# Kernel optimization log

Measured on AMD Instinct MI355X. Metric: run time of the kernel, lower is better.

The kernel has to match this reference:

```python
import jax, jax.numpy as jnp
import numpy as np

N, E, F, HID, PC, HEADS = 100000, 1600000, 128, 128, 16, 4
RATIO = 0.8
NEG_SLOPE = 0.2
BIG_NEG = -1e9


def setup_inputs() -> dict:
    ks = jax.random.split(jax.random.key(0), 20)
    def g(k, shape, fan):
        return jax.random.normal(k, shape, jnp.float32) / np.float32(np.sqrt(fan))
    return {
        "x": jax.random.normal(ks[0], (N, F), jnp.float32),
        "edge_index": jax.random.randint(ks[1], (2, E), 0, N, dtype=jnp.int32),
        "edge_attr": jax.random.uniform(ks[2], (E, 1), dtype=jnp.float32),
        "W1": g(ks[3], (F, PC), F),
        "att_src1": g(ks[4], (HEADS, PC // HEADS), PC // HEADS),
        "att_dst1": g(ks[5], (HEADS, PC // HEADS), PC // HEADS),
        "We1": g(ks[6], (1, PC), 1),
        "att_edge1": g(ks[7], (HEADS, PC // HEADS), PC // HEADS),
        "b1": jnp.zeros((PC,), jnp.float32),
        "Wrel": g(ks[8], (PC, 1), PC),
        "brel": jnp.zeros((1,), jnp.float32),
        "Wroot": g(ks[9], (PC, 1), PC),
        "W2": g(ks[10], (PC, HID), PC),
        "att_src2": g(ks[11], (1, HID), HID),
        "att_dst2": g(ks[12], (1, HID), HID),
        "We2": g(ks[13], (1, HID), 1),
        "att_edge2": g(ks[14], (1, HID), HID),
        "b2": jnp.zeros((HID,), jnp.float32),
        "Wg": g(ks[15], (HID, 1), HID),
        "bg": jnp.zeros((1,), jnp.float32),
    }


def gat_conv(h_in, src, dst, e_attr, W, a_s, a_d, We, a_e, b, num_nodes, mask=None):
    """PyG GATConv (add_self_loops=False, eval-mode so dropout is identity)."""
    H, D = a_s.shape
    h = (h_in @ W).reshape(-1, H, D)                      # [N,H,D]
    al_s = jnp.einsum('nhd,hd->nh', h, a_s)               # alpha contribution of source
    al_d = jnp.einsum('nhd,hd->nh', h, a_d)               # alpha contribution of dest
    he = (e_attr @ We).reshape(-1, H, D)                  # [E,H,D] edge features
    al_e = jnp.einsum('ehd,hd->eh', he, a_e)              # [E,H]
    logits = jax.nn.leaky_relu(al_s[src] + al_d[dst] + al_e, NEG_SLOPE)  # [E,H]
    if mask is not None:
        logits = jnp.where(mask[:, None], logits, BIG_NEG)
    # segment softmax over incoming edges of each destination node
    m = jnp.maximum(jax.ops.segment_max(logits, dst, num_segments=num_nodes), BIG_NEG)
    num = jnp.exp(logits - m[dst])
    if mask is not None:
        num = jnp.where(mask[:, None], num, 0.0)
    den = jax.ops.segment_sum(num, dst, num_segments=num_nodes)
    coef = num / jnp.maximum(den[dst], 1e-16)             # [E,H]
    out = jax.ops.segment_sum(coef[:, :, None] * h[src], dst, num_segments=num_nodes)
    return out.reshape(num_nodes, H * D) + b


def _forward(x, edge_attr, W1, att_src1, att_dst1, We1, att_edge1, b1,
             Wrel, brel, Wroot, W2, att_src2, att_dst2, We2, att_edge2, b2,
             Wg, bg, edge_index):
    n = x.shape[0]
    src, dst = edge_index[0], edge_index[1]
    h1 = jax.nn.relu(gat_conv(x, src, dst, edge_attr, W1, att_src1, att_dst1, We1, att_edge1, b1, n))
    # --- SAGPooling: GraphConv score -> tanh -> top-k -> masked subgraph (n > node_threshold always) ---
    agg = jax.ops.segment_sum(h1[src], dst, num_segments=n)           # neighbor sum
    score = (agg @ Wrel + brel + h1 @ Wroot).reshape(-1)              # GraphConv(16 -> 1)
    k = int(np.ceil(RATIO * n))                                       # static
    vals, perm = jax.lax.top_k(score, k)
    new_idx = jnp.full((n,), -1, dtype=jnp.int32).at[perm].set(jnp.arange(k, dtype=jnp.int32))
    src_n, dst_n = new_idx[src], new_idx[dst]
    emask = (src_n >= 0) & (dst_n >= 0)                               # edges with both ends kept
    src2 = jnp.where(emask, src_n, 0)
    dst2 = jnp.where(emask, dst_n, 0)
    x2 = h1[perm] * jnp.tanh(vals)[:, None]                           # gate kept nodes
    h2 = jax.nn.relu(gat_conv(x2, src2, dst2, edge_attr, W2, att_src2, att_dst2, We2, att_edge2, b2, k, mask=emask))
    # --- AttentionalAggregation + MaxAggregation over the single graph (index = zeros) ---
    gate = jax.nn.softmax(h2 @ Wg + bg, axis=0)                       # [k,1]
    att = (gate * h2).sum(axis=0, keepdims=True)                      # [1,HID]
    mx = h2.max(axis=0, keepdims=True)                                # [1,HID]
    return jnp.concatenate([att, mx], axis=1)                         # [1,2*HID]


def reference(x, edge_index, edge_attr, W1, att_src1, att_dst1, We1, att_edge1, b1,
              Wrel, brel, Wroot, W2, att_src2, att_dst2, We2, att_edge2, b2, Wg, bg):
    return _forward(x, edge_attr, W1, att_src1, att_dst1, We1, att_edge1, b1,
                    Wrel, brel, Wroot, W2, att_src2, att_dst2, We2, att_edge2, b2,
                    Wg, bg, edge_index)
```

## Files before the change

### kernel.cpp

```cpp
#include <hip/hip_runtime.h>
#include <hip/hip_bf16.h>

#define Nn 100000
#define Ee 1600000
#define Kk 80000
#define NB ((Nn + 255) / 256)
#define NBK 196
#define CHK 8192
#define G2B 2048

typedef unsigned int uint;
typedef unsigned short ushort;

struct Scal {
    uint prefix, remaining, needEq;
    float c1[4];
    float c2;
    uint gmaxOrd;
    float deng;
    float attnum[128];
    uint mxOrd[128];
};

__device__ __forceinline__ uint f2ord(float f) {
    uint b = __float_as_uint(f);
    return (b & 0x80000000u) ? ~b : (b | 0x80000000u);
}
__device__ __forceinline__ float ord2f(uint u) {
    uint b = (u & 0x80000000u) ? (u ^ 0x80000000u) : ~u;
    return __uint_as_float(b);
}
__device__ __forceinline__ float lrelu(float v) { return v > 0.f ? v : 0.2f * v; }
__device__ __forceinline__ float2 bf2f2(uint u) {
    return make_float2(__uint_as_float(u << 16), __uint_as_float(u & 0xFFFF0000u));
}

__global__ __launch_bounds__(256) void initK(uint* bcnt, uint* hist, Scal* sc,
                                             const float* We1, const float* ae1,
                                             const float* We2, const float* ae2) {
    int i = blockIdx.x * 256 + threadIdx.x;
    if (i < NBK) bcnt[i] = 0u;
    if (i < 256) hist[i] = 0u;
    if (i < 128) { sc->attnum[i] = 0.f; sc->mxOrd[i] = f2ord(0.0f); }
    if (i == 0) {
        sc->prefix = 0u; sc->remaining = Kk; sc->needEq = 0u;
        sc->deng = 0.f; sc->gmaxOrd = f2ord(-1e30f);
        for (int h = 0; h < 4; h++) {
            float s = 0.f;
            for (int d = 0; d < 4; d++) s += We1[h * 4 + d] * ae1[h * 4 + d];
            sc->c1[h] = s;
        }
        float s2 = 0.f;
        for (int d = 0; d < 128; d++) s2 += We2[d] * ae2[d];
        sc->c2 = s2;
    }
}

__global__ __launch_bounds__(256) void nodeL1(const float* __restrict__ x,
                                              const float* __restrict__ W1,
                                              const float* __restrict__ as1,
                                              const float* __restrict__ ad1,
                                              float* __restrict__ hpre,
                                              float* __restrict__ alS1,
                                              float* __restrict__ alD1) {
    __shared__ float Ws[128 * 16];
    __shared__ float s_as[16], s_ad[16];
    for (int i = threadIdx.x; i < 2048; i += 256) Ws[i] = W1[i];
    if (threadIdx.x < 16) { s_as[threadIdx.x] = as1[threadIdx.x]; s_ad[threadIdx.x] = ad1[threadIdx.x]; }
    __syncthreads();
    int n = blockIdx.x * 256 + threadIdx.x;
    if (n >= Nn) return;
    float acc[16];
#pragma unroll
    for (int j = 0; j < 16; j++) acc[j] = 0.f;
    const float4* xr = (const float4*)(x + (size_t)n * 128);
    for (int t4 = 0; t4 < 32; t4++) {
        float4 xv = xr[t4];
#pragma unroll
        for (int j = 0; j < 16; j++) {
            acc[j] += xv.x * Ws[(t4 * 4 + 0) * 16 + j];
            acc[j] += xv.y * Ws[(t4 * 4 + 1) * 16 + j];
            acc[j] += xv.z * Ws[(t4 * 4 + 2) * 16 + j];
            acc[j] += xv.w * Ws[(t4 * 4 + 3) * 16 + j];
        }
    }
    float* hp = hpre + (size_t)n * 16;
#pragma unroll
    for (int j = 0; j < 16; j++) hp[j] = acc[j];
#pragma unroll
    for (int h = 0; h < 4; h++) {
        float s = 0.f, d = 0.f;
#pragma unroll
        for (int q = 0; q < 4; q++) {
            s += acc[h * 4 + q] * s_as[h * 4 + q];
            d += acc[h * 4 + q] * s_ad[h * 4 + q];
        }
        alS1[n * 4 + h] = s;
        alD1[n * 4 + h] = d;
    }
}

__global__ __launch_bounds__(256) void bucketCnt(const int* __restrict__ ei, uint* __restrict__ bcnt) {
    __shared__ uint h[NBK];
    if (threadIdx.x < NBK) h[threadIdx.x] = 0u;
    __syncthreads();
    for (int e = blockIdx.x * 256 + threadIdx.x; e < Ee; e += gridDim.x * 256)
        atomicAdd(&h[((uint)ei[Ee + e]) >> 9], 1u);
    __syncthreads();
    if (threadIdx.x < NBK && h[threadIdx.x]) atomicAdd(&bcnt[threadIdx.x], h[threadIdx.x]);
}

__global__ __launch_bounds__(256) void scanBk(const uint* __restrict__ bcnt, uint* __restrict__ boff,
                                              uint* __restrict__ gcur) {
    __shared__ uint s[256];
    int t = threadIdx.x;
    uint v = (t < NBK) ? bcnt[t] : 0u;
    s[t] = v;
    __syncthreads();
    for (int off = 1; off < 256; off <<= 1) {
        uint u = (t >= off) ? s[t - off] : 0u;
        __syncthreads();
        s[t] += u;
        __syncthreads();
    }
    if (t < NBK) { boff[t] = s[t] - v; gcur[t] = 0u; }
    if (t == 0) boff[NBK] = Ee;
}

__global__ __launch_bounds__(256) void binScat(const int* __restrict__ ei, const float* __restrict__ ea,
                                               const uint* __restrict__ boff, uint* __restrict__ gcur,
                                               uint2* __restrict__ bsE, ushort* __restrict__ bsD) {
    __shared__ uint h[NBK], base[NBK], h2[NBK];
    int t = threadIdx.x;
    if (t < NBK) h[t] = 0u;
    __syncthreads();
    int estart = blockIdx.x * CHK;
    int eend = min(Ee, estart + CHK);
    for (int e = estart + t; e < eend; e += 256)
        atomicAdd(&h[((uint)ei[Ee + e]) >> 9], 1u);
    __syncthreads();
    if (t < NBK) { base[t] = atomicAdd(&gcur[t], h[t]); h2[t] = 0u; }
    __syncthreads();
    for (int e = estart + t; e < eend; e += 256) {
        uint d = (uint)ei[Ee + e];
        uint b = d >> 9;
        uint r = atomicAdd(&h2[b], 1u);
        uint pos = boff[b] + base[b] + r;
        bsE[pos] = make_uint2((uint)ei[e], __float_as_uint(ea[e]));
        bsD[pos] = (ushort)(d & 511u);
    }
}

__global__ __launch_bounds__(256) void rankK(const uint* __restrict__ boff, const ushort* __restrict__ bsD,
                                             ushort* __restrict__ bsR, uint* __restrict__ deg) {
    __shared__ uint ldeg[512];
    int b = blockIdx.x, t = threadIdx.x;
    ldeg[t] = 0u; ldeg[t + 256] = 0u;
    __syncthreads();
    uint r0 = boff[b], r1 = boff[b + 1];
    for (uint i = r0 + t; i < r1; i += 256)
        bsR[i] = (ushort)atomicAdd(&ldeg[bsD[i]], 1u);
    __syncthreads();
    int nd = b * 512 + t;
    if (nd < Nn) deg[nd] = ldeg[t];
    nd = b * 512 + 256 + t;
    if (nd < Nn) deg[nd] = ldeg[256 + t];
}

__global__ __launch_bounds__(256) void scanA(const uint* __restrict__ deg, uint* __restrict__ rowstart,
                                             uint* __restrict__ blkSum) {
    __shared__ uint s[256];
    int i = blockIdx.x * 256 + threadIdx.x;
    uint v = (i < Nn) ? deg[i] : 0u;
    s[threadIdx.x] = v;
    __syncthreads();
    for (int off = 1; off < 256; off <<= 1) {
        uint t = (threadIdx.x >= off) ? s[threadIdx.x - off] : 0u;
        __syncthreads();
        s[threadIdx.x] += t;
        __syncthreads();
    }
    if (i < Nn) rowstart[i] = s[threadIdx.x] - v;
    if (threadIdx.x == 255) blkSum[blockIdx.x] = s[255];
}

__global__ __launch_bounds__(512) void scanB(const uint* __restrict__ blkSum, uint* __restrict__ blkOff) {
    __shared__ uint s[512];
    uint v = (threadIdx.x < NB) ? blkSum[threadIdx.x] : 0u;
    s[threadIdx.x] = v;
    __syncthreads();
    for (int off = 1; off < 512; off <<= 1) {
        uint t = (threadIdx.x >= off) ? s[threadIdx.x - off] : 0u;
        __syncthreads();
        s[threadIdx.x] += t;
        __syncthreads();
    }
    if (threadIdx.x < NB) blkOff[threadIdx.x] = s[threadIdx.x] - v;
}

__global__ __launch_bounds__(256) void scanC(uint* __restrict__ rowstart, const uint* __restrict__ blkOff) {
    int i = blockIdx.x * 256 + threadIdx.x;
    if (i < Nn) rowstart[i] += blkOff[blockIdx.x];
    if (i == 0) rowstart[Nn] = Ee;
}

__global__ __launch_bounds__(256) void placeK(const uint* __restrict__ boff, const uint2* __restrict__ bsE,
                                              const ushort* __restrict__ bsD, const ushort* __restrict__ bsR,
                                              const uint* __restrict__ rowstart, uint2* __restrict__ csr_p8) {
    __shared__ uint srs[512];
    int b = blockIdx.x, t = threadIdx.x;
    int nd = b * 512 + t;
    srs[t] = (nd < Nn) ? rowstart[nd] : 0u;
    nd = b * 512 + 256 + t;
    srs[256 + t] = (nd < Nn) ? rowstart[nd] : 0u;
    __syncthreads();
    uint r0 = boff[b], r1 = boff[b + 1];
    for (uint i = r0 + t; i < r1; i += 256)
        csr_p8[srs[bsD[i]] + bsR[i]] = bsE[i];
}

__global__ __launch_bounds__(256) void gather1f(const uint2* __restrict__ csr_p8,
                                                const uint* __restrict__ rowstart,
                                                const float* __restrict__ alS1, const float* __restrict__ alD1,
                                                const float* __restrict__ hpre, const Scal* __restrict__ scc,
                                                const float* __restrict__ b1, const float* __restrict__ Wrel,
                                                const float* __restrict__ Wroot,
                                                float* __restrict__ h1, float* __restrict__ p,
                                                float* __restrict__ q) {
    int tid = blockIdx.x * 256 + threadIdx.x;
    if (tid >= Nn * 4) return;
    int d = tid >> 2, h = tid & 3;
    uint r0 = rowstart[d], r1 = rowstart[d + 1];
    float ad = alD1[tid];
    float c1h = scc->c1[h];
    float den = 0.f;
    float4 acc = {0.f, 0.f, 0.f, 0.f};
#pragma unroll 8
    for (uint i = r0; i < r1; i++) {
        uint2 p8 = csr_p8[i];
        int s = (int)p8.x;
        float e = __expf(lrelu(alS1[s * 4 + h] + __uint_as_float(p8.y) * c1h + ad));
        float4 hv = *(const float4*)(hpre + (size_t)s * 16 + h * 4);
        den += e;
        acc.x += e * hv.x; acc.y += e * hv.y;
        acc.z += e * hv.z; acc.w += e * hv.w;
    }
    float inv = 1.f / fmaxf(den, 1e-16f);
    float4 o;
    o.x = fmaxf(acc.x * inv + b1[h * 4 + 0], 0.f);
    o.y = fmaxf(acc.y * inv + b1[h * 4 + 1], 0.f);
    o.z = fmaxf(acc.z * inv + b1[h * 4 + 2], 0.f);
    o.w = fmaxf(acc.w * inv + b1[h * 4 + 3], 0.f);
    *(float4*)(h1 + (size_t)d * 16 + h * 4) = o;
    float pp = o.x * Wrel[h * 4 + 0] + o.y * Wrel[h * 4 + 1] + o.z * Wrel[h * 4 + 2] + o.w * Wrel[h * 4 + 3];
    float qq = o.x * Wroot[h * 4 + 0] + o.y * Wroot[h * 4 + 1] + o.z * Wroot[h * 4 + 2] + o.w * Wroot[h * 4 + 3];
    pp += __shfl_xor(pp, 1); pp += __shfl_xor(pp, 2);
    qq += __shfl_xor(qq, 1); qq += __shfl_xor(qq, 2);
    if (h == 0) { p[d] = pp; q[d] = qq; }
}

__global__ __launch_bounds__(256) void scoreK2(const uint2* __restrict__ csr_p8, const uint* __restrict__ rowstart,
                                               const float* __restrict__ p, const float* __restrict__ q,
                                               const float* __restrict__ brel,
                                               float* __restrict__ score, uint* __restrict__ dkey) {
    int d = blockIdx.x * 256 + threadIdx.x;
    if (d >= Nn) return;
    uint r0 = rowstart[d], r1 = rowstart[d + 1];
    float s = brel[0] + q[d];
#pragma unroll 8
    for (uint i = r0; i < r1; i++) s += p[(int)csr_p8[i].x];
    score[d] = s;
    dkey[d] = ~f2ord(s);
}

__global__ __launch_bounds__(256) void histK(const uint* __restrict__ dkey, const Scal* __restrict__ sc,
                                             uint* __restrict__ hist, int shift) {
    __shared__ uint lh[256];
    lh[threadIdx.x] = 0u;
    __syncthreads();
    int i = blockIdx.x * 256 + threadIdx.x;
    if (i < Nn) {
        uint d = dkey[i];
        bool ok = (shift == 24) || ((d >> (shift + 8)) == sc->prefix);
        if (ok) atomicAdd(&lh[(d >> shift) & 255u], 1u);
    }
    __syncthreads();
    if (lh[threadIdx.x]) atomicAdd(&hist[threadIdx.x], lh[threadIdx.x]);
}

__global__ __launch_bounds__(256) void selP(Scal* sc, uint* hist) {
    __shared__ uint s[256];
    int t = threadIdx.x;
    uint c = hist[t];
    s[t] = c;
    __syncthreads();
    for (int off = 1; off < 256; off <<= 1) {
        uint v = (t >= off) ? s[t - off] : 0u;
        __syncthreads();
        s[t] += v;
        __syncthreads();
    }
    uint rem = sc->remaining;
    uint cum = s[t];
    uint cumex = cum - c;
    if (cum >= rem && cumex < rem) {
        sc->remaining = rem - cumex;
        sc->prefix = (sc->prefix << 8) | (uint)t;
    }
    hist[t] = 0u;
}

__global__ __launch_bounds__(256) void cntK(const uint* __restrict__ dkey, const Scal* __restrict__ sc,
                                            uint* __restrict__ blkLt, uint* __restrict__ blkEq) {
    int i = blockIdx.x * 256 + threadIdx.x;
    uint ut = sc->prefix;
    bool lt = (i < Nn) && (dkey[i] < ut);
    bool eq = (i < Nn) && (dkey[i] == ut);
    __shared__ uint sl[4], se[4];
    unsigned long long bl = __ballot(lt), be = __ballot(eq);
    int lane = threadIdx.x & 63, w = threadIdx.x >> 6;
    if (lane == 0) { sl[w] = (uint)__popcll(bl); se[w] = (uint)__popcll(be); }
    __syncthreads();
    if (threadIdx.x == 0) {
        blkLt[blockIdx.x] = sl[0] + sl[1] + sl[2] + sl[3];
        blkEq[blockIdx.x] = se[0] + se[1] + se[2] + se[3];
    }
}

__global__ __launch_bounds__(512) void prefP(Scal* sc, const uint* __restrict__ blkLt,
                                             const uint* __restrict__ blkEq, uint* __restrict__ eqPref) {
    __shared__ uint se[512];
    __shared__ uint sl[512];
    int t = threadIdx.x;
    uint e = (t < NB) ? blkEq[t] : 0u;
    uint l = (t < NB) ? blkLt[t] : 0u;
    se[t] = e; sl[t] = l;
    __syncthreads();
    for (int off = 1; off < 512; off <<= 1) {
        uint v1 = (t >= off) ? se[t - off] : 0u;
        uint v2 = (t >= off) ? sl[t - off] : 0u;
        __syncthreads();
        se[t] += v1; sl[t] += v2;
        __syncthreads();
    }
    if (t < NB) eqPref[t] = se[t] - e;
    if (t == 511) sc->needEq = Kk - sl[511];
}

__global__ __launch_bounds__(256) void keptK(const uint* __restrict__ dkey, const Scal* __restrict__ sc,
                                             const uint* __restrict__ eqPref, int* __restrict__ kept) {
    int i = blockIdx.x * 256 + threadIdx.x;
    uint ut = sc->prefix, needEq = sc->needEq;
    bool inr = i < Nn;
    uint d = inr ? dkey[i] : 0xFFFFFFFFu;
    bool isLt = inr && (d < ut);
    bool isEq = inr && (d == ut);
    __shared__ uint wcnt[4];
    unsigned long long mask = __ballot(isEq);
    int lane = threadIdx.x & 63, w = threadIdx.x >> 6;
    uint lanePre = (uint)__popcll(mask & ((1ull << lane) - 1ull));
    if (lane == 0) wcnt[w] = (uint)__popcll(mask);
    __syncthreads();
    uint wo = 0;
    for (int q = 0; q < 4; q++) if (q < w) wo += wcnt[q];
    uint rank = eqPref[blockIdx.x] + wo + lanePre;
    if (inr) kept[i] = (isLt || (isEq && rank < needEq)) ? 1 : 0;
}

__global__ __launch_bounds__(256) void nodeL2(const float* __restrict__ h1, const float* __restrict__ score,
                                              const int* __restrict__ kept, const float* __restrict__ W2,
                                              const float* __restrict__ as2, const float* __restrict__ ad2,
                                              __hip_bfloat162* __restrict__ h2b, float* __restrict__ alS2k,
                                              float* __restrict__ alD2) {
    __shared__ float Ws[16 * 128];
    for (int i = threadIdx.x; i < 2048; i += 256) Ws[i] = W2[i];
    __syncthreads();
    int wid = (blockIdx.x * 256 + threadIdx.x) >> 6;
    int lane = threadIdx.x & 63;
    if (wid >= Nn) return;
    int n = wid;
    if (!kept[n]) { if (lane == 0) alS2k[n] = -1e30f; return; }
    float t = tanhf(score[n]);
    float x2[16];
    const float* hr = h1 + (size_t)n * 16;
#pragma unroll
    for (int j = 0; j < 16; j++) x2[j] = hr[j] * t;
    int d0 = 2 * lane, d1 = 2 * lane + 1;
    float a0 = 0.f, a1 = 0.f;
    const float2* Wv = (const float2*)Ws;
#pragma unroll
    for (int j = 0; j < 16; j++) {
        float2 wv = Wv[j * 64 + lane];
        a0 += x2[j] * wv.x;
        a1 += x2[j] * wv.y;
    }
    __hip_bfloat162 hb;
    hb.x = __float2bfloat16(a0);
    hb.y = __float2bfloat16(a1);
    h2b[(size_t)n * 64 + lane] = hb;
    float s = a0 * as2[d0] + a1 * as2[d1];
    float dd = a0 * ad2[d0] + a1 * ad2[d1];
#pragma unroll
    for (int off = 32; off; off >>= 1) { s += __shfl_xor(s, off); dd += __shfl_xor(dd, off); }
    if (lane == 0) { alS2k[n] = s; alD2[n] = dd; }
}

__global__ __launch_bounds__(256) void gather2g(const uint2* __restrict__ csr_p8,
                                                const uint* __restrict__ rowstart, const int* __restrict__ kept,
                                                const float* __restrict__ alS2k, const float* __restrict__ alD2,
                                                const Scal* __restrict__ scc,
                                                const __hip_bfloat162* __restrict__ h2b, const float* __restrict__ b2,
                                                const float* __restrict__ Wg, const float* __restrict__ bg,
                                                float* __restrict__ pacc, float* __restrict__ pmx,
                                                float* __restrict__ pden) {
    __shared__ float sAtt[4][16][8];
    __shared__ float sMx[4][16][8];
    __shared__ float sDen[4];
    int w = threadIdx.x >> 6, lane = threadIdx.x & 63;
    int g = lane >> 4, t = lane & 15;
    float4 b2a = ((const float4*)b2)[t * 2], b2b = ((const float4*)b2)[t * 2 + 1];
    float4 wga = ((const float4*)Wg)[t * 2], wgb = ((const float4*)Wg)[t * 2 + 1];
    float bg0 = bg[0];
    float c2 = scc->c2;
    const uint* h2u = (const uint*)h2b;
    float att[8], mx8[8], denP = 0.f;
#pragma unroll
    for (int j = 0; j < 8; j++) { att[j] = 0.f; mx8[j] = 0.f; }
    for (int n = blockIdx.x * 4 + w; n < Nn; n += G2B * 4) {
        if (!kept[n]) continue;
        float ad = alD2[n];
        uint r0 = rowstart[n];
        uint len = rowstart[n + 1] - r0;
        float den = 0.f;
        float acc[8];
#pragma unroll
        for (int d = 0; d < 8; d++) acc[d] = 0.f;
#pragma unroll 2
        for (uint base = 0; base < len; base += 4) {
            uint off = base + (uint)g;
            bool act = off < len;
            uint sidx = act ? (r0 + off) : (r0 + len - 1);
            uint2 p8 = csr_p8[sidx];
            int s = (int)p8.x;
            float pv = alS2k[s] + __uint_as_float(p8.y) * c2;
            pv = act ? pv : -1e30f;
            float c = __expf(lrelu(pv + ad));
            uint4 hv = *(const uint4*)(h2u + (size_t)s * 64 + t * 4);
            den += c;
            float2 f;
            f = bf2f2(hv.x); acc[0] += c * f.x; acc[1] += c * f.y;
            f = bf2f2(hv.y); acc[2] += c * f.x; acc[3] += c * f.y;
            f = bf2f2(hv.z); acc[4] += c * f.x; acc[5] += c * f.y;
            f = bf2f2(hv.w); acc[6] += c * f.x; acc[7] += c * f.y;
        }
#pragma unroll
        for (int d = 0; d < 8; d++) {
            acc[d] += __shfl_xor(acc[d], 16);
            acc[d] += __shfl_xor(acc[d], 32);
        }
        den += __shfl_xor(den, 16);
        den += __shfl_xor(den, 32);
        float inv = 1.f / fmaxf(den, 1e-16f);
        float o[8];
        o[0] = fmaxf(acc[0] * inv + b2a.x, 0.f);
        o[1] = fmaxf(acc[1] * inv + b2a.y, 0.f);
        o[2] = fmaxf(acc[2] * inv + b2a.z, 0.f);
        o[3] = fmaxf(acc[3] * inv + b2a.w, 0.f);
        o[4] = fmaxf(acc[4] * inv + b2b.x, 0.f);
        o[5] = fmaxf(acc[5] * inv + b2b.y, 0.f);
        o[6] = fmaxf(acc[6] * inv + b2b.z, 0.f);
        o[7] = fmaxf(acc[7] * inv + b2b.w, 0.f);
        float gp = o[0] * wga.x + o[1] * wga.y + o[2] * wga.z + o[3] * wga.w +
                   o[4] * wgb.x + o[5] * wgb.y + o[6] * wgb.z + o[7] * wgb.w;
#pragma unroll
        for (int off = 8; off; off >>= 1) gp += __shfl_xor(gp, off);
        float e = __expf(gp + bg0);
        denP += e;
#pragma unroll
        for (int j = 0; j < 8; j++) {
            att[j] += e * o[j];
            mx8[j] = fmaxf(mx8[j], o[j]);
        }
    }
    if (g == 0) {
#pragma unroll
        for (int j = 0; j < 8; j++) { sAtt[w][t][j] = att[j]; sMx[w][t][j] = mx8[j]; }
    }
    if (lane == 0) sDen[w] = denP;
    __syncthreads();
    int tid = threadIdx.x;
    if (tid < 128) {
        int tt = tid >> 3, j = tid & 7;
        float a = sAtt[0][tt][j] + sAtt[1][tt][j] + sAtt[2][tt][j] + sAtt[3][tt][j];
        float m = fmaxf(fmaxf(sMx[0][tt][j], sMx[1][tt][j]), fmaxf(sMx[2][tt][j], sMx[3][tt][j]));
        pacc[(size_t)blockIdx.x * 128 + tid] = a;
        pmx[(size_t)blockIdx.x * 128 + tid] = m;
    }
    if (tid == 0) pden[blockIdx.x] = sDen[0] + sDen[1] + sDen[2] + sDen[3];
}

__global__ __launch_bounds__(256) void gateRed(const float* __restrict__ pacc, const float* __restrict__ pmx,
                                               const float* __restrict__ pden, Scal* sc) {
    __shared__ float r[256];
    int b = blockIdx.x, tid = threadIdx.x;
    if (b < 128) {
        float a = 0.f, m = 0.f;
        for (int i = tid; i < G2B; i += 256) {
            a += pacc[(size_t)i * 128 + b];
            m = fmaxf(m, pmx[(size_t)i * 128 + b]);
        }
        r[tid] = a;
        __syncthreads();
        for (int off = 128; off; off >>= 1) {
            if (tid < off) r[tid] += r[tid + off];
            __syncthreads();
        }
        float asum = r[0];
        __syncthreads();
        r[tid] = m;
        __syncthreads();
        for (int off = 128; off; off >>= 1) {
            if (tid < off) r[tid] = fmaxf(r[tid], r[tid + off]);
            __syncthreads();
        }
        if (tid == 0) { sc->attnum[b] = asum; sc->mxOrd[b] = f2ord(r[0]); }
    } else {
        float d = 0.f;
        for (int i = tid; i < G2B; i += 256) d += pden[i];
        r[tid] = d;
        __syncthreads();
        for (int off = 128; off; off >>= 1) {
            if (tid < off) r[tid] += r[tid + off];
            __syncthreads();
        }
        if (tid == 0) sc->deng = r[0];
    }
}

__global__ void outK(const Scal* sc, float* out) {
    int d = threadIdx.x;
    if (d < 128) {
        out[d] = sc->attnum[d] / sc->deng;
        out[128 + d] = ord2f(sc->mxOrd[d]);
    }
}

extern "C" void kernel_launch(void* const* d_in, const int* in_sizes, int n_in,
                              void* d_out, int out_size, void* d_ws, size_t ws_size,
                              hipStream_t stream) {
    const float* x = (const float*)d_in[0];
    const int* ei = (const int*)d_in[1];
    const float* ea = (const float*)d_in[2];
    const float* W1 = (const float*)d_in[3];
    const float* as1 = (const float*)d_in[4];
    const float* ad1 = (const float*)d_in[5];
    const float* We1 = (const float*)d_in[6];
    const float* ae1 = (const float*)d_in[7];
    const float* b1 = (const float*)d_in[8];
    const float* Wrel = (const float*)d_in[9];
    const float* brel = (const float*)d_in[10];
    const float* Wroot = (const float*)d_in[11];
    const float* W2 = (const float*)d_in[12];
    const float* as2 = (const float*)d_in[13];
    const float* ad2 = (const float*)d_in[14];
    const float* We2 = (const float*)d_in[15];
    const float* ae2 = (const float*)d_in[16];
    const float* b2 = (const float*)d_in[17];
    const float* Wg = (const float*)d_in[18];
    const float* bg = (const float*)d_in[19];
    float* out = (float*)d_out;

    float* base = (float*)d_ws;
    size_t o = 0;
    auto alloc = [&](size_t nf) { float* p2 = base + o; o += nf; return p2; };
    uint2* bsE = (uint2*)alloc((size_t)Ee * 2);
    ushort* bsD = (ushort*)alloc((size_t)Ee / 2);
    ushort* bsR = (ushort*)alloc((size_t)Ee / 2);
    uint2* csr_p8 = (uint2*)alloc((size_t)Ee * 2);
    __hip_bfloat162* h2b = (__hip_bfloat162*)alloc((size_t)Nn * 64);
    float* hpre = alloc((size_t)Nn * 16);
    float* h1 = alloc((size_t)Nn * 16);
    float* pacc = alloc((size_t)G2B * 128);
    float* pmx = alloc((size_t)G2B * 128);
    float* pden = alloc(G2B);
    float* alS1 = alloc((size_t)Nn * 4);
    float* alD1 = alloc((size_t)Nn * 4);
    float* p = alloc(Nn);
    float* q = alloc(Nn);
    float* score = alloc(Nn);
    uint* dkey = (uint*)alloc(Nn);
    uint* deg = (uint*)alloc(Nn);
    int* kept = (int*)alloc(Nn);
    float* alS2k = alloc(Nn);
    float* alD2 = alloc(Nn);
    uint* rowstart = (uint*)alloc(Nn + 1);
    uint* hist = (uint*)alloc(256);
    uint* blkSum = (uint*)alloc(NB);
    uint* blkOff = (uint*)alloc(NB);
    uint* blkLt = (uint*)alloc(NB);
    uint* blkEq = (uint*)alloc(NB);
    uint* eqPref = (uint*)alloc(NB);
    uint* bcnt = (uint*)alloc(NBK);
    uint* boff = (uint*)alloc(NBK + 1);
    uint* gcur = (uint*)alloc(NBK);
    Scal* sc = (Scal*)alloc(512);

    auto cdiv = [](long a, long b) { return (int)((a + b - 1) / b); };

    initK<<<NB, 256, 0, stream>>>(bcnt, hist, sc, We1, ae1, We2, ae2);
    nodeL1<<<NB, 256, 0, stream>>>(x, W1, as1, ad1, hpre, alS1, alD1);
    bucketCnt<<<512, 256, 0, stream>>>(ei, bcnt);
    scanBk<<<1, 256, 0, stream>>>(bcnt, boff, gcur);
    binScat<<<cdiv(Ee, CHK), 256, 0, stream>>>(ei, ea, boff, gcur, bsE, bsD);
    rankK<<<NBK, 256, 0, stream>>>(boff, bsD, bsR, deg);
    scanA<<<NB, 256, 0, stream>>>(deg, rowstart, blkSum);
    scanB<<<1, 512, 0, stream>>>(blkSum, blkOff);
    scanC<<<NB, 256, 0, stream>>>(rowstart, blkOff);
    placeK<<<NBK, 256, 0, stream>>>(boff, bsE, bsD, bsR, rowstart, csr_p8);
    gather1f<<<cdiv((long)Nn * 4, 256), 256, 0, stream>>>(csr_p8, rowstart, alS1, alD1, hpre, sc,
                                                          b1, Wrel, Wroot, h1, p, q);
    scoreK2<<<NB, 256, 0, stream>>>(csr_p8, rowstart, p, q, brel, score, dkey);
    for (int shift = 24; shift >= 0; shift -= 8) {
        histK<<<NB, 256, 0, stream>>>(dkey, sc, hist, shift);
        selP<<<1, 256, 0, stream>>>(sc, hist);
    }
    cntK<<<NB, 256, 0, stream>>>(dkey, sc, blkLt, blkEq);
    prefP<<<1, 512, 0, stream>>>(sc, blkLt, blkEq, eqPref);
    keptK<<<NB, 256, 0, stream>>>(dkey, sc, eqPref, kept);
    nodeL2<<<cdiv(Nn, 4), 256, 0, stream>>>(h1, score, kept, W2, as2, ad2, h2b, alS2k, alD2);
    gather2g<<<G2B, 256, 0, stream>>>(csr_p8, rowstart, kept, alS2k, alD2, sc,
                                      h2b, b2, Wg, bg, pacc, pmx, pden);
    gateRed<<<129, 256, 0, stream>>>(pacc, pmx, pden, sc);
    outK<<<1, 128, 0, stream>>>(sc, out);
}
```

Baseline: 342.5 us.

## Fuse CSR rank/scan/place into one kernel and fold first radix histogram into scoring

Replaces the rankK, three-stage global scan and placeK sequence with a single per-bucket kernel. It counts degrees in shared memory, does a local scan offset by the bucket base, and places edges directly. This drops the bsR and deg intermediate buffers and four kernel launches. The first top-k radix histogram pass is folded into the scoring kernel. The gather2g inner loop unroll is also raised from 2 to 4. Risks: placement order inside a row now depends on shared atomic order, and one block per bucket does all the work serially.

```diff
diff --git a/kernel.cpp b/kernel.cpp
--- a/kernel.cpp
+++ b/kernel.cpp
@@ -151,72 +151,45 @@
     }
 }
 
-__global__ __launch_bounds__(256) void rankK(const uint* __restrict__ boff, const ushort* __restrict__ bsD,
-                                             ushort* __restrict__ bsR, uint* __restrict__ deg) {
+__global__ __launch_bounds__(256) void rankPlace(const uint* __restrict__ boff, const uint2* __restrict__ bsE,
+                                                 const ushort* __restrict__ bsD,
+                                                 uint2* __restrict__ csr_p8, uint* __restrict__ rowstart) {
     __shared__ uint ldeg[512];
+    __shared__ uint lscan[512];
+    __shared__ uint ps[256];
     int b = blockIdx.x, t = threadIdx.x;
     ldeg[t] = 0u; ldeg[t + 256] = 0u;
     __syncthreads();
     uint r0 = boff[b], r1 = boff[b + 1];
     for (uint i = r0 + t; i < r1; i += 256)
-        bsR[i] = (ushort)atomicAdd(&ldeg[bsD[i]], 1u);
-    __syncthreads();
+        atomicAdd(&ldeg[bsD[i]], 1u);
+    __syncthreads();
+    uint pv = ldeg[2 * t] + ldeg[2 * t + 1];
+    ps[t] = pv;
+    __syncthreads();
+    for (int off = 1; off < 256; off <<= 1) {
+        uint u = (t >= off) ? ps[t - off] : 0u;
+        __syncthreads();
+        ps[t] += u;
+        __syncthreads();
+    }
+    uint pbase = ps[t] - pv;
+    lscan[2 * t] = pbase;
+    lscan[2 * t + 1] = pbase + ldeg[2 * t];
+    __syncthreads();
+    uint bb = boff[b];
     int nd = b * 512 + t;
-    if (nd < Nn) deg[nd] = ldeg[t];
+    if (nd < Nn) rowstart[nd] = bb + lscan[t];
     nd = b * 512 + 256 + t;
-    if (nd < Nn) deg[nd] = ldeg[256 + t];
-}
-
-__global__ __launch_bounds__(256) void scanA(const uint* __restrict__ deg, uint* __restrict__ rowstart,
-                                             uint* __restrict__ blkSum) {
-    __shared__ uint s[256];
-    int i = blockIdx.x * 256 + threadIdx.x;
-    uint v = (i < Nn) ? deg[i] : 0u;
-    s[threadIdx.x] = v;
-    __syncthreads();
-    for (int off = 1; off < 256; off <<= 1) {
-        uint t = (threadIdx.x >= off) ? s[threadIdx.x - off] : 0u;
-        __syncthreads();
-        s[threadIdx.x] += t;
-        __syncthreads();
-    }
-    if (i < Nn) rowstart[i] = s[threadIdx.x] - v;
-    if (threadIdx.x == 255) blkSum[blockIdx.x] = s[255];
-}
-
-__global__ __launch_bounds__(512) void scanB(const uint* __restrict__ blkSum, uint* __restrict__ blkOff) {
-    __shared__ uint s[512];
-    uint v = (threadIdx.x < NB) ? blkSum[threadIdx.x] : 0u;
-    s[threadIdx.x] = v;
-    __syncthreads();
-    for (int off = 1; off < 512; off <<= 1) {
-        uint t = (threadIdx.x >= off) ? s[threadIdx.x - off] : 0u;
-        __syncthreads();
-        s[threadIdx.x] += t;
-        __syncthreads();
-    }
-    if (threadIdx.x < NB) blkOff[threadIdx.x] = s[threadIdx.x] - v;
-}
-
-__global__ __launch_bounds__(256) void scanC(uint* __restrict__ rowstart, const uint* __restrict__ blkOff) {
-    int i = blockIdx.x * 256 + threadIdx.x;
-    if (i < Nn) rowstart[i] += blkOff[blockIdx.x];
-    if (i == 0) rowstart[Nn] = Ee;
-}
-
-__global__ __launch_bounds__(256) void placeK(const uint* __restrict__ boff, const uint2* __restrict__ bsE,
-                                              const ushort* __restrict__ bsD, const ushort* __restrict__ bsR,
-                                              const uint* __restrict__ rowstart, uint2* __restrict__ csr_p8) {
-    __shared__ uint srs[512];
-    int b = blockIdx.x, t = threadIdx.x;
-    int nd = b * 512 + t;
-    srs[t] = (nd < Nn) ? rowstart[nd] : 0u;
-    nd = b * 512 + 256 + t;
-    srs[256 + t] = (nd < Nn) ? rowstart[nd] : 0u;
-    __syncthreads();
-    uint r0 = boff[b], r1 = boff[b + 1];
-    for (uint i = r0 + t; i < r1; i += 256)
-        csr_p8[srs[bsD[i]] + bsR[i]] = bsE[i];
+    if (nd < Nn) rowstart[nd] = bb + lscan[256 + t];
+    if (b == 0 && t == 0) rowstart[Nn] = Ee;
+    ldeg[t] = 0u; ldeg[t + 256] = 0u;
+    __syncthreads();
+    for (uint i = r0 + t; i < r1; i += 256) {
+        ushort dl = bsD[i];
+        uint r = atomicAdd(&ldeg[dl], 1u);
+        csr_p8[bb + lscan[dl] + r] = bsE[i];
+    }
 }
 
 __global__ __launch_bounds__(256) void gather1f(const uint2* __restrict__ csr_p8,
@@ -259,18 +232,27 @@
     if (h == 0) { p[d] = pp; q[d] = qq; }
 }
 
-__global__ __launch_bounds__(256) void scoreK2(const uint2* __restrict__ csr_p8, const uint* __restrict__ rowstart,
-                                               const float* __restrict__ p, const float* __restrict__ q,
-                                               const float* __restrict__ brel,
-                                               float* __restrict__ score, uint* __restrict__ dkey) {
+__global__ __launch_bounds__(256) void scoreH(const uint2* __restrict__ csr_p8, const uint* __restrict__ rowstart,
+                                              const float* __restrict__ p, const float* __restrict__ q,
+                                              const float* __restrict__ brel,
+                                              float* __restrict__ score, uint* __restrict__ dkey,
+                                              uint* __restrict__ hist) {
+    __shared__ uint lh[256];
+    lh[threadIdx.x] = 0u;
+    __syncthreads();
     int d = blockIdx.x * 256 + threadIdx.x;
-    if (d >= Nn) return;
-    uint r0 = rowstart[d], r1 = rowstart[d + 1];
-    float s = brel[0] + q[d];
+    if (d < Nn) {
+        uint r0 = rowstart[d], r1 = rowstart[d + 1];
+        float s = brel[0] + q[d];
 #pragma unroll 8
-    for (uint i = r0; i < r1; i++) s += p[(int)csr_p8[i].x];
-    score[d] = s;
-    dkey[d] = ~f2ord(s);
+        for (uint i = r0; i < r1; i++) s += p[(int)csr_p8[i].x];
+        score[d] = s;
+        uint k = ~f2ord(s);
+        dkey[d] = k;
+        atomicAdd(&lh[k >> 24], 1u);
+    }
+    __syncthreads();
+    if (lh[threadIdx.x]) atomicAdd(&hist[threadIdx.x], lh[threadIdx.x]);
 }
 
 __global__ __launch_bounds__(256) void histK(const uint* __restrict__ dkey, const Scal* __restrict__ sc,
@@ -281,8 +263,7 @@
     int i = blockIdx.x * 256 + threadIdx.x;
     if (i < Nn) {
         uint d = dkey[i];
-        bool ok = (shift == 24) || ((d >> (shift + 8)) == sc->prefix);
-        if (ok) atomicAdd(&lh[(d >> shift) & 255u], 1u);
+        if ((d >> (shift + 8)) == sc->prefix) atomicAdd(&lh[(d >> shift) & 255u], 1u);
     }
     __syncthreads();
     if (lh[threadIdx.x]) atomicAdd(&hist[threadIdx.x], lh[threadIdx.x]);
@@ -362,7 +343,7 @@
     if (lane == 0) wcnt[w] = (uint)__popcll(mask);
     __syncthreads();
     uint wo = 0;
-    for (int q = 0; q < 4; q++) if (q < w) wo += wcnt[q];
+    for (int qq = 0; qq < 4; qq++) if (qq < w) wo += wcnt[qq];
     uint rank = eqPref[blockIdx.x] + wo + lanePre;
     if (inr) kept[i] = (isLt || (isEq && rank < needEq)) ? 1 : 0;
 }
@@ -435,7 +416,7 @@
         float acc[8];
 #pragma unroll
         for (int d = 0; d < 8; d++) acc[d] = 0.f;
-#pragma unroll 2
+#pragma unroll 4
         for (uint base = 0; base < len; base += 4) {
             uint off = base + (uint)g;
             bool act = off < len;
@@ -575,7 +556,6 @@
     auto alloc = [&](size_t nf) { float* p2 = base + o; o += nf; return p2; };
     uint2* bsE = (uint2*)alloc((size_t)Ee * 2);
     ushort* bsD = (ushort*)alloc((size_t)Ee / 2);
-    ushort* bsR = (ushort*)alloc((size_t)Ee / 2);
     uint2* csr_p8 = (uint2*)alloc((size_t)Ee * 2);
     __hip_bfloat162* h2b = (__hip_bfloat162*)alloc((size_t)Nn * 64);
     float* hpre = alloc((size_t)Nn * 16);
@@ -589,14 +569,11 @@
     float* q = alloc(Nn);
     float* score = alloc(Nn);
     uint* dkey = (uint*)alloc(Nn);
-    uint* deg = (uint*)alloc(Nn);
     int* kept = (int*)alloc(Nn);
     float* alS2k = alloc(Nn);
     float* alD2 = alloc(Nn);
     uint* rowstart = (uint*)alloc(Nn + 1);
     uint* hist = (uint*)alloc(256);
-    uint* blkSum = (uint*)alloc(NB);
-    uint* blkOff = (uint*)alloc(NB);
     uint* blkLt = (uint*)alloc(NB);
     uint* blkEq = (uint*)alloc(NB);
     uint* eqPref = (uint*)alloc(NB);
@@ -612,15 +589,12 @@
     bucketCnt<<<512, 256, 0, stream>>>(ei, bcnt);
     scanBk<<<1, 256, 0, stream>>>(bcnt, boff, gcur);
     binScat<<<cdiv(Ee, CHK), 256, 0, stream>>>(ei, ea, boff, gcur, bsE, bsD);
-    rankK<<<NBK, 256, 0, stream>>>(boff, bsD, bsR, deg);
-    scanA<<<NB, 256, 0, stream>>>(deg, rowstart, blkSum);
-    scanB<<<1, 512, 0, stream>>>(blkSum, blkOff);
-    scanC<<<NB, 256, 0, stream>>>(rowstart, blkOff);
-    placeK<<<NBK, 256, 0, stream>>>(boff, bsE, bsD, bsR, rowstart, csr_p8);
+    rankPlace<<<NBK, 256, 0, stream>>>(boff, bsE, bsD, csr_p8, rowstart);
     gather1f<<<cdiv((long)Nn * 4, 256), 256, 0, stream>>>(csr_p8, rowstart, alS1, alD1, hpre, sc,
                                                           b1, Wrel, Wroot, h1, p, q);
-    scoreK2<<<NB, 256, 0, stream>>>(csr_p8, rowstart, p, q, brel, score, dkey);
-    for (int shift = 24; shift >= 0; shift -= 8) {
+    scoreH<<<NB, 256, 0, stream>>>(csr_p8, rowstart, p, q, brel, score, dkey, hist);
+    selP<<<1, 256, 0, stream>>>(sc, hist);
+    for (int shift = 16; shift >= 0; shift -= 8) {
         histK<<<NB, 256, 0, stream>>>(dkey, sc, hist, shift);
         selP<<<1, 256, 0, stream>>>(sc, hist);
     }
```

Result: faster. 334.8 us (-2.2%).
